# Optimization experiments

Hardware: AMD Instinct MI355X
Metric: run time of the kernel (lower is better)

The kernel has to match this reference:

```python
import jax, jax.numpy as jnp
import numpy as np

N = 8192
SPIKE_THRESHOLD = 30.0
E_L0, TAU_M0, TAU_G0 = -50.0, 1.8, 2.7
W_MEAN, W_VAR = 0.3, 0.2


def setup_inputs() -> dict:
    key = jax.random.key(0)
    k1, k2, k3, k4 = jax.random.split(key, 4)
    x_in = jax.random.uniform(k1, (N,), dtype=jnp.float32)
    # membrane potential near resting potential E_L
    v = E_L0 + 2.0 * jax.random.normal(k2, (N,), dtype=jnp.float32)
    g = jax.random.uniform(k3, (N,), dtype=jnp.float32)
    # weights: uniform in [w_mean - w_var, w_mean + w_var], then signed per neuron type
    w = W_MEAN - W_VAR + 2.0 * W_VAR * jax.random.uniform(k4, (N, N), dtype=jnp.float32)
    sign = jnp.concatenate([jnp.ones(N // 2), -jnp.ones(N // 2)]).astype(jnp.float32)
    w = jnp.abs(w) * sign[:, None]  # excitatory rows +, inhibitory rows -
    E_L = jnp.full((N,), E_L0, dtype=jnp.float32)
    tau_m = jnp.full((N,), TAU_M0, dtype=jnp.float32)
    tau_g = jnp.full((N,), TAU_G0, dtype=jnp.float32)
    return {"x_in": x_in, "v": v, "g": g, "w": w, "E_L": E_L, "tau_m": tau_m, "tau_g": tau_g}


def reference(x_in, v, g, w, E_L, tau_m, tau_g):
    # synaptic input: I_j = sum_i g_i * w_ij  (vector-matrix product)
    I = g @ w  # [N]
    I = jax.nn.sigmoid(2.0 * 6.0 * I / N) + 0.9 * x_in
    norm_R_f = SPIKE_THRESHOLD - E_L
    v_next = v + (E_L - v + I * norm_R_f) / tau_m  # [N]
    spiked_soft = jax.nn.sigmoid(v_next - SPIKE_THRESHOLD)
    return spiked_soft
```

## Files before the change

kernel.cpp:

```cpp
#include <hip/hip_runtime.h>
#include <hip/hip_bf16.h>

#define NN 8192

typedef float f32x4 __attribute__((ext_vector_type(4)));

__global__ __launch_bounds__(256) void lif_gemv_part(
    const float* __restrict__ g, const float* __restrict__ w,
    float* __restrict__ partial, int rows_per_split)
{
    const int col = blockIdx.x * 1024 + threadIdx.x * 4;
    const int s   = blockIdx.y;
    const int r0  = s * rows_per_split;

    const float* wp = w + (size_t)r0 * NN + col;
    const float* gp = g + r0;

    f32x4 acc = {0.f, 0.f, 0.f, 0.f};
    #pragma unroll 8
    for (int i = 0; i < rows_per_split; ++i) {
        const float gi = gp[i];
        const f32x4 wv = *reinterpret_cast<const f32x4*>(wp + (size_t)i * NN);
        acc.x = fmaf(gi, wv.x, acc.x);
        acc.y = fmaf(gi, wv.y, acc.y);
        acc.z = fmaf(gi, wv.z, acc.z);
        acc.w = fmaf(gi, wv.w, acc.w);
    }
    *reinterpret_cast<f32x4*>(partial + (size_t)s * NN + col) = acc;
}

__device__ __forceinline__ float lif_activation(
    float I, float x, float vv, float el, float tm)
{
    const float arg   = 12.0f * I / 8192.0f;
    const float Isig  = 1.0f / (1.0f + expf(-arg));
    const float Ifull = Isig + 0.9f * x;
    const float v_next = vv + (el - vv + Ifull * (30.0f - el)) / tm;
    return 1.0f / (1.0f + expf(30.0f - v_next));
}

template <int S>
__global__ __launch_bounds__(256) void lif_pointwise_t(
    const float* __restrict__ partial,
    const float* __restrict__ x_in, const float* __restrict__ v,
    const float* __restrict__ E_L, const float* __restrict__ tau_m,
    float* __restrict__ out)
{
    const int cl = threadIdx.x & 31;
    const int kg = threadIdx.x >> 5;
    const int j  = blockIdx.x * 32 + cl;
    constexpr int PER = S / 8;

    float acc = 0.f;
    #pragma unroll
    for (int s = 0; s < PER; ++s)
        acc += partial[(size_t)(kg * PER + s) * NN + j];

    __shared__ float red[8][32];
    red[kg][cl] = acc;
    __syncthreads();

    if (threadIdx.x < 32) {
        float I = red[0][cl];
        #pragma unroll
        for (int k = 1; k < 8; ++k) I += red[k][cl];
        out[j] = lif_activation(I, x_in[j], v[j], E_L[j], tau_m[j]);
    }
}

__global__ __launch_bounds__(256) void lif_pointwise_rt(
    const float* __restrict__ partial, int nsplits,
    const float* __restrict__ x_in, const float* __restrict__ v,
    const float* __restrict__ E_L, const float* __restrict__ tau_m,
    float* __restrict__ out)
{
    const int j = blockIdx.x * blockDim.x + threadIdx.x;
    if (j >= NN) return;
    float I = 0.f;
    for (int s = 0; s < nsplits; ++s)
        I += partial[(size_t)s * NN + j];
    out[j] = lif_activation(I, x_in[j], v[j], E_L[j], tau_m[j]);
}

extern "C" void kernel_launch(void* const* d_in, const int* in_sizes, int n_in,
                              void* d_out, int out_size, void* d_ws, size_t ws_size,
                              hipStream_t stream) {
    const float* x_in  = (const float*)d_in[0];
    const float* v     = (const float*)d_in[1];
    const float* g     = (const float*)d_in[2];
    const float* w     = (const float*)d_in[3];
    const float* E_L   = (const float*)d_in[4];
    const float* tau_m = (const float*)d_in[5];
    float* out     = (float*)d_out;
    float* partial = (float*)d_ws;

    int S = 128;
    while (S > 1 && (size_t)S * NN * sizeof(float) > ws_size) S >>= 1;

    dim3 grid1(NN / 1024, S);
    lif_gemv_part<<<grid1, 256, 0, stream>>>(g, w, partial, NN / S);

    switch (S) {
        case 128: lif_pointwise_t<128><<<NN / 32, 256, 0, stream>>>(partial, x_in, v, E_L, tau_m, out); break;
        case  64: lif_pointwise_t< 64><<<NN / 32, 256, 0, stream>>>(partial, x_in, v, E_L, tau_m, out); break;
        case  32: lif_pointwise_t< 32><<<NN / 32, 256, 0, stream>>>(partial, x_in, v, E_L, tau_m, out); break;
        default:  lif_pointwise_rt<<<NN / 256, 256, 0, stream>>>(partial, S, x_in, v, E_L, tau_m, out); break;
    }
}
```

Baseline: 50.00 us.

## Use 256-way row split GEMV with full-width 1024-thread blocks

Adds a GEMV kernel where each of 256 blocks of 1024 threads covers a contiguous 32-row slab across all 8192 columns, each thread loading two float4s per row. This makes each block stream a contiguous 1 MB region, aiming for better DRAM streaming than the old column-tiled split. In exchange, the partial buffer doubles to 256 rows (8 MB), which means more partial-sum write and reduce traffic in the pointwise kernel. The old path is kept as a fallback when the workspace is too small.

```diff
diff --git a/kernel.cpp b/kernel.cpp
--- a/kernel.cpp
+++ b/kernel.cpp
@@ -4,30 +4,6 @@
 #define NN 8192
 
 typedef float f32x4 __attribute__((ext_vector_type(4)));
-
-__global__ __launch_bounds__(256) void lif_gemv_part(
-    const float* __restrict__ g, const float* __restrict__ w,
-    float* __restrict__ partial, int rows_per_split)
-{
-    const int col = blockIdx.x * 1024 + threadIdx.x * 4;
-    const int s   = blockIdx.y;
-    const int r0  = s * rows_per_split;
-
-    const float* wp = w + (size_t)r0 * NN + col;
-    const float* gp = g + r0;
-
-    f32x4 acc = {0.f, 0.f, 0.f, 0.f};
-    #pragma unroll 8
-    for (int i = 0; i < rows_per_split; ++i) {
-        const float gi = gp[i];
-        const f32x4 wv = *reinterpret_cast<const f32x4*>(wp + (size_t)i * NN);
-        acc.x = fmaf(gi, wv.x, acc.x);
-        acc.y = fmaf(gi, wv.y, acc.y);
-        acc.z = fmaf(gi, wv.z, acc.z);
-        acc.w = fmaf(gi, wv.w, acc.w);
-    }
-    *reinterpret_cast<f32x4*>(partial + (size_t)s * NN + col) = acc;
-}
 
 __device__ __forceinline__ float lif_activation(
     float I, float x, float vv, float el, float tm)
@@ -37,6 +13,37 @@
     const float Ifull = Isig + 0.9f * x;
     const float v_next = vv + (el - vv + Ifull * (30.0f - el)) / tm;
     return 1.0f / (1.0f + expf(30.0f - v_next));
+}
+
+__global__ __launch_bounds__(1024) void lif_gemv_seq(
+    const float* __restrict__ g, const float* __restrict__ w,
+    float* __restrict__ partial)
+{
+    const int b  = blockIdx.x;
+    const int t  = threadIdx.x;
+    const int r0 = b * 32;
+
+    const float* wp = w + (size_t)r0 * NN + t * 4;
+    const float* gp = g + r0;
+
+    f32x4 acc0 = {0.f, 0.f, 0.f, 0.f};
+    f32x4 acc1 = {0.f, 0.f, 0.f, 0.f};
+    #pragma unroll 4
+    for (int i = 0; i < 32; ++i) {
+        const float gi = gp[i];
+        const f32x4 w0 = *reinterpret_cast<const f32x4*>(wp + (size_t)i * NN);
+        const f32x4 w1 = *reinterpret_cast<const f32x4*>(wp + (size_t)i * NN + 4096);
+        acc0.x = fmaf(gi, w0.x, acc0.x);
+        acc0.y = fmaf(gi, w0.y, acc0.y);
+        acc0.z = fmaf(gi, w0.z, acc0.z);
+        acc0.w = fmaf(gi, w0.w, acc0.w);
+        acc1.x = fmaf(gi, w1.x, acc1.x);
+        acc1.y = fmaf(gi, w1.y, acc1.y);
+        acc1.z = fmaf(gi, w1.z, acc1.z);
+        acc1.w = fmaf(gi, w1.w, acc1.w);
+    }
+    *reinterpret_cast<f32x4*>(partial + (size_t)b * NN + t * 4)        = acc0;
+    *reinterpret_cast<f32x4*>(partial + (size_t)b * NN + 4096 + t * 4) = acc1;
 }
 
 template <int S>
@@ -68,6 +75,28 @@
     }
 }
 
+__global__ __launch_bounds__(256) void lif_gemv_part_rt(
+    const float* __restrict__ g, const float* __restrict__ w,
+    float* __restrict__ partial, int rps)
+{
+    const int col = blockIdx.x * 1024 + threadIdx.x * 4;
+    const int s   = blockIdx.y;
+    const int r0  = s * rps;
+    const float* wp = w + (size_t)r0 * NN + col;
+    const float* gp = g + r0;
+    f32x4 acc = {0.f, 0.f, 0.f, 0.f};
+    #pragma unroll 8
+    for (int i = 0; i < rps; ++i) {
+        const float gi = gp[i];
+        const f32x4 wv = *reinterpret_cast<const f32x4*>(wp + (size_t)i * NN);
+        acc.x = fmaf(gi, wv.x, acc.x);
+        acc.y = fmaf(gi, wv.y, acc.y);
+        acc.z = fmaf(gi, wv.z, acc.z);
+        acc.w = fmaf(gi, wv.w, acc.w);
+    }
+    *reinterpret_cast<f32x4*>(partial + (size_t)s * NN + col) = acc;
+}
+
 __global__ __launch_bounds__(256) void lif_pointwise_rt(
     const float* __restrict__ partial, int nsplits,
     const float* __restrict__ x_in, const float* __restrict__ v,
@@ -94,16 +123,21 @@
     float* out     = (float*)d_out;
     float* partial = (float*)d_ws;
 
-    int S = 128;
-    while (S > 1 && (size_t)S * NN * sizeof(float) > ws_size) S >>= 1;
+    constexpr size_t SEQ_BYTES = (size_t)256 * NN * sizeof(float);
 
-    dim3 grid1(NN / 1024, S);
-    lif_gemv_part<<<grid1, 256, 0, stream>>>(g, w, partial, NN / S);
-
-    switch (S) {
-        case 128: lif_pointwise_t<128><<<NN / 32, 256, 0, stream>>>(partial, x_in, v, E_L, tau_m, out); break;
-        case  64: lif_pointwise_t< 64><<<NN / 32, 256, 0, stream>>>(partial, x_in, v, E_L, tau_m, out); break;
-        case  32: lif_pointwise_t< 32><<<NN / 32, 256, 0, stream>>>(partial, x_in, v, E_L, tau_m, out); break;
-        default:  lif_pointwise_rt<<<NN / 256, 256, 0, stream>>>(partial, S, x_in, v, E_L, tau_m, out); break;
+    if (ws_size >= SEQ_BYTES) {
+        lif_gemv_seq<<<256, 1024, 0, stream>>>(g, w, partial);
+        lif_pointwise_t<256><<<NN / 32, 256, 0, stream>>>(partial, x_in, v, E_L, tau_m, out);
+    } else {
+        int S = 128;
+        while (S > 1 && (size_t)S * NN * sizeof(float) > ws_size) S >>= 1;
+        dim3 grid1(NN / 1024, S);
+        lif_gemv_part_rt<<<grid1, 256, 0, stream>>>(g, w, partial, NN / S);
+        switch (S) {
+            case 128: lif_pointwise_t<128><<<NN / 32, 256, 0, stream>>>(partial, x_in, v, E_L, tau_m, out); break;
+            case  64: lif_pointwise_t< 64><<<NN / 32, 256, 0, stream>>>(partial, x_in, v, E_L, tau_m, out); break;
+            case  32: lif_pointwise_t< 32><<<NN / 32, 256, 0, stream>>>(partial, x_in, v, E_L, tau_m, out); break;
+            default:  lif_pointwise_rt<<<NN / 256, 256, 0, stream>>>(partial, S, x_in, v, E_L, tau_m, out); break;
+        }
     }
 }
```

Result: slower. 60.41 us (+20.8%).
